# Performance work log

Measured on AMD Instinct MI355X. Metric: run time of the kernel, lower is better.

The kernel has to match this reference:

```python
import jax, jax.numpy as jnp
import numpy as np

N = 50000
E = 640000
H = 128


def setup_inputs() -> dict:
    key = jax.random.key(0)
    ks = jax.random.split(key, 16)
    s = 0.02
    return {
        "x": jax.random.uniform(ks[0], (N, 1), dtype=jnp.float32),
        "pre_h": jax.random.normal(ks[1], (N, H), dtype=jnp.float32),
        "edge_index": jax.random.randint(ks[2], (2, E), 0, N, dtype=jnp.int32),
        "edge_attr": jax.random.uniform(ks[3], (E, 1), dtype=jnp.float32),
        # encoder: Linear(1+H, H)
        "W_enc": jax.random.normal(ks[4], (1 + H, H), dtype=jnp.float32) * s,
        "b_enc": jnp.zeros((H,), dtype=jnp.float32),
        # message: Linear(2H+1, H)
        "W_M": jax.random.normal(ks[5], (2 * H + 1, H), dtype=jnp.float32) * s,
        "b_M": jnp.zeros((H,), dtype=jnp.float32),
        # update: Linear(2H, H)
        "W_U": jax.random.normal(ks[6], (2 * H, H), dtype=jnp.float32) * s,
        "b_U": jnp.zeros((H,), dtype=jnp.float32),
        # decoder: Linear(2H, 1)
        "W_dec": jax.random.normal(ks[7], (2 * H, 1), dtype=jnp.float32) * s,
        "b_dec": jnp.zeros((1,), dtype=jnp.float32),
        # terminator: Linear(2H, 1)
        "W_term": jax.random.normal(ks[8], (2 * H, 1), dtype=jnp.float32) * s,
        "b_term": jnp.zeros((1,), dtype=jnp.float32),
    }


def reference(x, pre_h, edge_index, edge_attr,
              W_enc, b_enc, W_M, b_M, W_U, b_U,
              W_dec, b_dec, W_term, b_term):
    n = x.shape[0]
    # Encoder: z = relu(Linear([x, pre_h]))  -> [N, H]
    z = jax.nn.relu(jnp.concatenate([x, pre_h], axis=-1) @ W_enc + b_enc)

    # MPNN processor (PyG flow source_to_target: row=src j, col=dst i)
    src, dst = edge_index[0], edge_index[1]
    z_i = z[dst]  # [E, H]
    z_j = z[src]  # [E, H]
    m = jax.nn.relu(jnp.concatenate([z_i, z_j, edge_attr], axis=-1) @ W_M + b_M)
    agg = jax.ops.segment_max(m, dst, num_segments=n)
    # PyG fills nodes with no incoming edges with 0 for max aggregation;
    # messages are >= 0 (relu) so clamping at 0 matches exactly.
    agg = jnp.maximum(agg, jnp.float32(0.0))
    h = jax.nn.relu(jnp.concatenate([z, agg], axis=-1) @ W_U + b_U)

    # Decoder: y = Linear([z, h]) -> [N, 1]
    y = jnp.concatenate([z, h], axis=-1) @ W_dec + b_dec

    # Terminator
    h_mean = jnp.mean(h, axis=0, keepdims=True)              # [1, H]
    hm = jnp.broadcast_to(h_mean, h.shape)                   # [N, H]
    t = jnp.concatenate([h, hm], axis=-1) @ W_term + b_term  # [N, 1]
    tau = jnp.mean(t, axis=0, keepdims=True)                 # [1, 1]

    return h, y, tau
```

## Files before the change

kernel.cpp:

```cpp
#include <hip/hip_runtime.h>

#define DEVINL __device__ __forceinline__
#define BCAP 64
#define NREP 64

typedef __attribute__((ext_vector_type(8))) short short8;
typedef __attribute__((ext_vector_type(4))) float f32x4;
typedef __attribute__((ext_vector_type(4))) unsigned short ushort4v;

DEVINL unsigned short f2bf(float f) {
    unsigned u = __float_as_uint(f);
    u += 0x7fffu + ((u >> 16) & 1u);
    return (unsigned short)(u >> 16);
}
DEVINL float bf2f(unsigned short s) { return __uint_as_float(((unsigned)s) << 16); }

__global__ __launch_bounds__(256) void k_w(
    const float* __restrict__ Wenc, const float* __restrict__ WM,
    const float* __restrict__ WU,
    unsigned short* __restrict__ WencT, unsigned short* __restrict__ WM1T,
    unsigned short* __restrict__ WM2T, unsigned short* __restrict__ WUT,
    int* __restrict__ zbase, int zn)
{
    if (blockIdx.x < 64) {
        int tid = blockIdx.x * 256 + threadIdx.x;
        const int nt = 64 * 256;
        for (int i = tid; i < 128 * 128; i += nt) {
            int c = i >> 7, k = i & 127;
            WencT[c * 128 + k] = f2bf(Wenc[(1 + k) * 128 + c]);
            WM1T[c * 128 + k]  = f2bf(WM[k * 128 + c]);
            WM2T[c * 128 + k]  = f2bf(WM[(128 + k) * 128 + c]);
        }
        for (int i = tid; i < 128 * 256; i += nt) {
            int c = i >> 8, k = i & 255;
            WUT[c * 256 + k] = f2bf(WU[k * 128 + c]);
        }
    } else {
        for (int i = (blockIdx.x - 64) * 256 + threadIdx.x; i < zn; i += 32 * 256)
            zbase[i] = 0;
    }
}


__global__ __launch_bounds__(256) void k_zq(
    const float* __restrict__ x, const float* __restrict__ preh,
    const unsigned short* __restrict__ WencT, const float* __restrict__ Wenc,
    const float* __restrict__ benc, const unsigned short* __restrict__ WM2T,
    unsigned short* __restrict__ zb, unsigned short* __restrict__ Qb,
    int N, int nzq,
    const int* __restrict__ ei, const float* __restrict__ attr,
    int* __restrict__ cnt, int2* __restrict__ bucket, int E)
{
    if ((int)blockIdx.x >= nzq) {
        int e = ((int)blockIdx.x - nzq) * 256 + threadIdx.x;
        if (e >= E) return;
        int src = ei[e];
        int dst = ei[E + e];
        float a = attr[e];
        int slot = atomicAdd(&cnt[dst], 1);
        if (slot < BCAP)
            bucket[(size_t)dst * BCAP + slot] = make_int2(src, __float_as_int(a));
        return;
    }
    __shared__ __align__(16) unsigned short zl[16][136];
    int t = threadIdx.x;
    int wave = t >> 6, lane = t & 63;
    int m = lane & 15, quad = lane >> 4;
    int node = (int)blockIdx.x * 16 + m;
    bool valid = node < N;
    int nodec = min(node, N - 1);
    f32x4 acc[2] = {(f32x4)0.f, (f32x4)0.f};
    const float* arow = preh + (size_t)nodec * 128;
#pragma unroll
    for (int kc = 0; kc < 4; ++kc) {
        int k0 = kc * 32 + quad * 8;
        float4 f0 = *(const float4*)(arow + k0);
        float4 f1 = *(const float4*)(arow + k0 + 4);
        short8 bfrag;
        bfrag[0] = (short)f2bf(f0.x); bfrag[1] = (short)f2bf(f0.y);
        bfrag[2] = (short)f2bf(f0.z); bfrag[3] = (short)f2bf(f0.w);
        bfrag[4] = (short)f2bf(f1.x); bfrag[5] = (short)f2bf(f1.y);
        bfrag[6] = (short)f2bf(f1.z); bfrag[7] = (short)f2bf(f1.w);
#pragma unroll
        for (int tt = 0; tt < 2; ++tt) {
            int t8 = wave * 2 + tt;
            short8 afrag = *(const short8*)(WencT + (size_t)(t8 * 16 + m) * 128 + k0);
            acc[tt] = __builtin_amdgcn_mfma_f32_16x16x32_bf16(afrag, bfrag, acc[tt], 0, 0, 0);
        }
    }
    float xv = x[nodec];
#pragma unroll
    for (int tt = 0; tt < 2; ++tt) {
        int col = (wave * 2 + tt) * 16 + quad * 4;
        float4 w0v = *(const float4*)(Wenc + col);
        float4 bv  = *(const float4*)(benc + col);
        ushort4v o;
        o[0] = f2bf(fmaxf(acc[tt][0] + xv * w0v.x + bv.x, 0.f));
        o[1] = f2bf(fmaxf(acc[tt][1] + xv * w0v.y + bv.y, 0.f));
        o[2] = f2bf(fmaxf(acc[tt][2] + xv * w0v.z + bv.z, 0.f));
        o[3] = f2bf(fmaxf(acc[tt][3] + xv * w0v.w + bv.w, 0.f));
        if (valid) *(ushort4v*)(zb + (size_t)node * 128 + col) = o;
        *(ushort4v*)&zl[m][col] = o;
    }
    __syncthreads();
    f32x4 aQ[2] = {(f32x4)0.f, (f32x4)0.f};
#pragma unroll
    for (int kc = 0; kc < 4; ++kc) {
        int k0 = kc * 32 + quad * 8;
        short8 bfrag = *(const short8*)&zl[m][k0];
#pragma unroll
        for (int tt = 0; tt < 2; ++tt) {
            int t8 = wave * 2 + tt;
            short8 a2 = *(const short8*)(WM2T + (size_t)(t8 * 16 + m) * 128 + k0);
            aQ[tt] = __builtin_amdgcn_mfma_f32_16x16x32_bf16(a2, bfrag, aQ[tt], 0, 0, 0);
        }
    }
    if (!valid) return;
    unsigned short* qrow = Qb + (size_t)node * 128;
#pragma unroll
    for (int tt = 0; tt < 2; ++tt) {
        int col = (wave * 2 + tt) * 16 + quad * 4;
        ushort4v oq;
        oq[0] = f2bf(aQ[tt][0]); oq[1] = f2bf(aQ[tt][1]);
        oq[2] = f2bf(aQ[tt][2]); oq[3] = f2bf(aQ[tt][3]);
        *(ushort4v*)(qrow + col) = oq;
    }
}

__global__ __launch_bounds__(256) void k_aggh(
    const unsigned short* __restrict__ zb, const unsigned short* __restrict__ Qb,
    const int2* __restrict__ bucket, const int* __restrict__ cnt,
    const float* __restrict__ w3, const float* __restrict__ bM,
    const unsigned short* __restrict__ WUT, const unsigned short* __restrict__ WM1T,
    const float* __restrict__ bU, const float* __restrict__ Wd,
    const float* __restrict__ bd,
    float* __restrict__ h, float* __restrict__ y, float* __restrict__ hsumR,
    int N)
{
    __shared__ int degs[16];
    __shared__ __align__(16) int2 eb[16][BCAP];
    __shared__ __align__(16) float mac[16][132];
    __shared__ float ys[4][16];
    __shared__ float hsb[128];
    unsigned short (*al)[136] = (unsigned short (*)[136])eb;

    int t = threadIdx.x;
    int bid16 = (int)blockIdx.x * 16;
    int wave = t >> 6, lane = t & 63;
    int m = lane & 15, quad = lane >> 4;
    int node = bid16 + m;
    bool valid = node < N;
    int nodec = min(node, N - 1);

    const unsigned short* arow = zb + (size_t)nodec * 128;
    short8 zfr[4];
#pragma unroll
    for (int kc = 0; kc < 4; ++kc)
        zfr[kc] = *(const short8*)(arow + kc * 32 + quad * 8);

    if (t < 16) degs[t] = min(cnt[min(bid16 + t, N - 1)], BCAP);
    __syncthreads();
    for (int idx = t; idx < 16 * BCAP; idx += 256) {
        int nd = idx >> 6, sl = idx & (BCAP - 1);
        if (sl < degs[nd])
            eb[nd][sl] = bucket[(size_t)min(bid16 + nd, N - 1) * BCAP + sl];
    }
    __syncthreads();
    {
        int il = t >> 4, c0 = (t & 15) * 8;
        int deg = degs[il];
        float w[8];
        {
            float4 wa = *(const float4*)(w3 + c0), wb = *(const float4*)(w3 + c0 + 4);
            w[0]=wa.x; w[1]=wa.y; w[2]=wa.z; w[3]=wa.w;
            w[4]=wb.x; w[5]=wb.y; w[6]=wb.z; w[7]=wb.w;
        }
        const float NI = __uint_as_float(0xff800000u);
        float a8[8];
#pragma unroll
        for (int u = 0; u < 8; ++u) a8[u] = NI;
        int j = 0;
        for (; j + 7 < deg; j += 8) {
            int2 e[8]; short8 q[8];
#pragma unroll
            for (int b = 0; b < 8; ++b) e[b] = eb[il][j + b];
#pragma unroll
            for (int b = 0; b < 8; ++b)
                q[b] = *(const short8*)(Qb + (size_t)e[b].x * 128 + c0);
#pragma unroll
            for (int b = 0; b < 8; ++b) {
                float a = __int_as_float(e[b].y);
#pragma unroll
                for (int u = 0; u < 8; ++u)
                    a8[u] = fmaxf(a8[u], fmaf(a, w[u], bf2f((unsigned short)q[b][u])));
            }
        }
        for (; j + 3 < deg; j += 4) {
            int2 e[4]; short8 q[4];
#pragma unroll
            for (int b = 0; b < 4; ++b) e[b] = eb[il][j + b];
#pragma unroll
            for (int b = 0; b < 4; ++b)
                q[b] = *(const short8*)(Qb + (size_t)e[b].x * 128 + c0);
#pragma unroll
            for (int b = 0; b < 4; ++b) {
                float a = __int_as_float(e[b].y);
#pragma unroll
                for (int u = 0; u < 8; ++u)
                    a8[u] = fmaxf(a8[u], fmaf(a, w[u], bf2f((unsigned short)q[b][u])));
            }
        }
        for (; j < deg; ++j) {
            int2 e0 = eb[il][j];
            float a = __int_as_float(e0.y);
            short8 q0 = *(const short8*)(Qb + (size_t)e0.x * 128 + c0);
#pragma unroll
            for (int u = 0; u < 8; ++u)
                a8[u] = fmaxf(a8[u], fmaf(a, w[u], bf2f((unsigned short)q0[u])));
        }
        *(f32x4*)&mac[il][c0]     = *(f32x4*)&a8[0];
        *(f32x4*)&mac[il][c0 + 4] = *(f32x4*)&a8[4];
    }
    __syncthreads();
    {
        f32x4 accP[2] = {(f32x4)0.f, (f32x4)0.f};
#pragma unroll
        for (int kc = 0; kc < 4; ++kc) {
            int k0 = kc * 32 + quad * 8;
#pragma unroll
            for (int tt = 0; tt < 2; ++tt) {
                int t8 = wave * 2 + tt;
                short8 afrag = *(const short8*)(WM1T + (size_t)(t8 * 16 + m) * 128 + k0);
                accP[tt] = __builtin_amdgcn_mfma_f32_16x16x32_bf16(afrag, zfr[kc], accP[tt], 0, 0, 0);
            }
        }
#pragma unroll
        for (int tt = 0; tt < 2; ++tt) {
            int col = (wave * 2 + tt) * 16 + quad * 4;
            float4 bmv = *(const float4*)(bM + col);
            float4 mv  = *(const float4*)&mac[m][col];
            ushort4v o;
            o[0] = f2bf(fmaxf(accP[tt][0] + bmv.x + mv.x, 0.f));
            o[1] = f2bf(fmaxf(accP[tt][1] + bmv.y + mv.y, 0.f));
            o[2] = f2bf(fmaxf(accP[tt][2] + bmv.z + mv.z, 0.f));
            o[3] = f2bf(fmaxf(accP[tt][3] + bmv.w + mv.w, 0.f));
            *(ushort4v*)&al[m][col] = o;
        }
    }
    __syncthreads();
    f32x4 acc[2] = {(f32x4)0.f, (f32x4)0.f};
    float py = 0.f;
#pragma unroll
    for (int kc = 0; kc < 8; ++kc) {
        int k0 = kc * 32 + quad * 8;
        short8 bfrag;
        if (kc < 4) {
            bfrag = zfr[kc];
            if (wave == 0) {
                float4 wa = *(const float4*)(Wd + k0);
                float4 wb = *(const float4*)(Wd + k0 + 4);
                py += bf2f((unsigned short)bfrag[0]) * wa.x
                    + bf2f((unsigned short)bfrag[1]) * wa.y
                    + bf2f((unsigned short)bfrag[2]) * wa.z
                    + bf2f((unsigned short)bfrag[3]) * wa.w
                    + bf2f((unsigned short)bfrag[4]) * wb.x
                    + bf2f((unsigned short)bfrag[5]) * wb.y
                    + bf2f((unsigned short)bfrag[6]) * wb.z
                    + bf2f((unsigned short)bfrag[7]) * wb.w;
            }
        } else {
            bfrag = *(const short8*)&al[m][(kc - 4) * 32 + quad * 8];
        }
#pragma unroll
        for (int tt = 0; tt < 2; ++tt) {
            int t8 = wave * 2 + tt;
            short8 afrag = *(const short8*)(WUT + (size_t)(t8 * 16 + m) * 256 + k0);
            acc[tt] = __builtin_amdgcn_mfma_f32_16x16x32_bf16(afrag, bfrag, acc[tt], 0, 0, 0);
        }
    }
    const float* Wdh = Wd + 128;
    float* orow = h + (size_t)nodec * 128;
#pragma unroll
    for (int tt = 0; tt < 2; ++tt) {
        int col = (wave * 2 + tt) * 16 + quad * 4;
        float4 bv = *(const float4*)(bU + col);
        float4 o;
        o.x = valid ? fmaxf(acc[tt][0] + bv.x, 0.f) : 0.f;
        o.y = valid ? fmaxf(acc[tt][1] + bv.y, 0.f) : 0.f;
        o.z = valid ? fmaxf(acc[tt][2] + bv.z, 0.f) : 0.f;
        o.w = valid ? fmaxf(acc[tt][3] + bv.w, 0.f) : 0.f;
        if (valid) *(float4*)(orow + col) = o;
        float4 wd = *(const float4*)(Wdh + col);
        py += o.x * wd.x + o.y * wd.y + o.z * wd.z + o.w * wd.w;
        float4 s = o;
#pragma unroll
        for (int mask = 1; mask <= 8; mask <<= 1) {
            s.x += __shfl_xor(s.x, mask, 64);
            s.y += __shfl_xor(s.y, mask, 64);
            s.z += __shfl_xor(s.z, mask, 64);
            s.w += __shfl_xor(s.w, mask, 64);
        }
        if (m == 0) *(float4*)&hsb[col] = s;
    }
    py += __shfl_xor(py, 16, 64);
    py += __shfl_xor(py, 32, 64);
    if (lane < 16) ys[wave][lane] = py;
    __syncthreads();
    if (t < 16 && bid16 + t < N)
        y[bid16 + t] = ys[0][t] + ys[1][t] + ys[2][t] + ys[3][t] + bd[0];
    if (t < 128)
        atomicAdd(&hsumR[((int)blockIdx.x & (NREP - 1)) * 128 + t], hsb[t]);
}

__global__ __launch_bounds__(128) void k_tau(
    const float* __restrict__ hsumR, const float* __restrict__ Wt,
    const float* __restrict__ bt, float* __restrict__ tau, int N)
{
    __shared__ float sd[128];
    int t = threadIdx.x;
    float s = 0.f;
#pragma unroll
    for (int r = 0; r < NREP; ++r) s += hsumR[r * 128 + t];
    float v = s * (1.f / (float)N) * (Wt[t] + Wt[128 + t]);
    sd[t] = v;
    __syncthreads();
    for (int o = 64; o > 0; o >>= 1) {
        if (t < o) sd[t] += sd[t + o];
        __syncthreads();
    }
    if (t == 0) tau[0] = sd[0] + bt[0];
}

extern "C" void kernel_launch(void* const* d_in, const int* in_sizes, int n_in,
                              void* d_out, int out_size, void* d_ws, size_t ws_size,
                              hipStream_t stream)
{
    const float* x     = (const float*)d_in[0];
    const float* preh  = (const float*)d_in[1];
    const int*   ei    = (const int*)d_in[2];
    const float* attr  = (const float*)d_in[3];
    const float* Wenc  = (const float*)d_in[4];
    const float* benc  = (const float*)d_in[5];
    const float* WM    = (const float*)d_in[6];
    const float* bM    = (const float*)d_in[7];
    const float* WU    = (const float*)d_in[8];
    const float* bU    = (const float*)d_in[9];
    const float* Wd    = (const float*)d_in[10];
    const float* bd    = (const float*)d_in[11];
    const float* Wterm = (const float*)d_in[12];
    const float* bterm = (const float*)d_in[13];
    int N = in_sizes[0];
    int E = in_sizes[3];

    char* wp = (char*)d_ws;
    unsigned short* zb    = (unsigned short*)wp; wp += (size_t)N * 128 * 2;
    unsigned short* Qb    = (unsigned short*)wp; wp += (size_t)N * 128 * 2;
    int2*           bucket= (int2*)wp;           wp += (size_t)N * BCAP * 8;
    int*            cnt   = (int*)wp;            wp += (size_t)N * 4;
    float*          hsumR = (float*)wp;          wp += NREP * 128 * 4;
    unsigned short* WencT = (unsigned short*)wp; wp += 128 * 128 * 2;
    unsigned short* WM1T  = (unsigned short*)wp; wp += 128 * 128 * 2;
    unsigned short* WM2T  = (unsigned short*)wp; wp += 128 * 128 * 2;
    unsigned short* WUT   = (unsigned short*)wp; wp += 128 * 256 * 2;

    float* hout = (float*)d_out;
    float* yout = hout + (size_t)N * 128;
    float* tau  = yout + N;

    int nb16 = (N + 15) / 16;
    int sb = (E + 255) / 256;
    int zn = N + NREP * 128;

    k_w<<<96, 256, 0, stream>>>(Wenc, WM, WU, WencT, WM1T, WM2T, WUT,
                                cnt, zn);
    k_zq<<<nb16 + sb, 256, 0, stream>>>(x, preh, WencT, Wenc, benc, WM2T,
                                        zb, Qb, N, nb16,
                                        ei, attr, cnt, bucket, E);
    k_aggh<<<nb16, 256, 0, stream>>>(zb, Qb, bucket, cnt, WM + 256 * 128, bM,
                                     WUT, WM1T, bU, Wd, bd,
                                     hout, yout, hsumR, N);
    k_tau<<<1, 128, 0, stream>>>(hsumR, Wterm, bterm, tau, N);
}
```

Baseline: 260.0 us.

## Pack edge buckets into 32-bit entries and move scatter into prep kernel

Edge bucket entries are packed into one 32-bit word (16-bit source index plus a bf16 edge attribute) instead of an int2. This halves bucket write and read traffic and the shared-memory staging size. The edge scatter moves from the z/Q kernel into the weight-prep kernel, and counter zeroing becomes a memset. In exchange, source indices above 65535 are unsupported and edge_attr is rounded to bf16, and an extra barrier is added because the output staging aliases the smaller edge buffer.

```diff
diff --git a/kernel.cpp b/kernel.cpp
--- a/kernel.cpp
+++ b/kernel.cpp
@@ -15,12 +15,13 @@
 }
 DEVINL float bf2f(unsigned short s) { return __uint_as_float(((unsigned)s) << 16); }
 
-__global__ __launch_bounds__(256) void k_w(
+__global__ __launch_bounds__(256) void k_prep(
     const float* __restrict__ Wenc, const float* __restrict__ WM,
     const float* __restrict__ WU,
     unsigned short* __restrict__ WencT, unsigned short* __restrict__ WM1T,
     unsigned short* __restrict__ WM2T, unsigned short* __restrict__ WUT,
-    int* __restrict__ zbase, int zn)
+    const int* __restrict__ ei, const float* __restrict__ attr,
+    int* __restrict__ cnt, unsigned* __restrict__ bucket, int E)
 {
     if (blockIdx.x < 64) {
         int tid = blockIdx.x * 256 + threadIdx.x;
@@ -36,32 +37,24 @@
             WUT[c * 256 + k] = f2bf(WU[k * 128 + c]);
         }
     } else {
-        for (int i = (blockIdx.x - 64) * 256 + threadIdx.x; i < zn; i += 32 * 256)
-            zbase[i] = 0;
-    }
-}
-
-
-__global__ __launch_bounds__(256) void k_zq(
-    const float* __restrict__ x, const float* __restrict__ preh,
-    const unsigned short* __restrict__ WencT, const float* __restrict__ Wenc,
-    const float* __restrict__ benc, const unsigned short* __restrict__ WM2T,
-    unsigned short* __restrict__ zb, unsigned short* __restrict__ Qb,
-    int N, int nzq,
-    const int* __restrict__ ei, const float* __restrict__ attr,
-    int* __restrict__ cnt, int2* __restrict__ bucket, int E)
-{
-    if ((int)blockIdx.x >= nzq) {
-        int e = ((int)blockIdx.x - nzq) * 256 + threadIdx.x;
+        int e = ((int)blockIdx.x - 64) * 256 + threadIdx.x;
         if (e >= E) return;
         int src = ei[e];
         int dst = ei[E + e];
         float a = attr[e];
         int slot = atomicAdd(&cnt[dst], 1);
         if (slot < BCAP)
-            bucket[(size_t)dst * BCAP + slot] = make_int2(src, __float_as_int(a));
-        return;
-    }
+            bucket[(size_t)dst * BCAP + slot] = ((unsigned)src << 16) | f2bf(a);
+    }
+}
+
+
+__global__ __launch_bounds__(256) void k_zq(
+    const float* __restrict__ x, const float* __restrict__ preh,
+    const unsigned short* __restrict__ WencT, const float* __restrict__ Wenc,
+    const float* __restrict__ benc, const unsigned short* __restrict__ WM2T,
+    unsigned short* __restrict__ zb, unsigned short* __restrict__ Qb, int N)
+{
     __shared__ __align__(16) unsigned short zl[16][136];
     int t = threadIdx.x;
     int wave = t >> 6, lane = t & 63;
@@ -129,7 +122,7 @@
 
 __global__ __launch_bounds__(256) void k_aggh(
     const unsigned short* __restrict__ zb, const unsigned short* __restrict__ Qb,
-    const int2* __restrict__ bucket, const int* __restrict__ cnt,
+    const unsigned* __restrict__ bucket, const int* __restrict__ cnt,
     const float* __restrict__ w3, const float* __restrict__ bM,
     const unsigned short* __restrict__ WUT, const unsigned short* __restrict__ WM1T,
     const float* __restrict__ bU, const float* __restrict__ Wd,
@@ -138,7 +131,7 @@
     int N)
 {
     __shared__ int degs[16];
-    __shared__ __align__(16) int2 eb[16][BCAP];
+    __shared__ __align__(16) unsigned eb[16][68];
     __shared__ __align__(16) float mac[16][132];
     __shared__ float ys[4][16];
     __shared__ float hsb[128];
@@ -181,39 +174,39 @@
         for (int u = 0; u < 8; ++u) a8[u] = NI;
         int j = 0;
         for (; j + 7 < deg; j += 8) {
-            int2 e[8]; short8 q[8];
+            unsigned e[8]; short8 q[8];
 #pragma unroll
             for (int b = 0; b < 8; ++b) e[b] = eb[il][j + b];
 #pragma unroll
             for (int b = 0; b < 8; ++b)
-                q[b] = *(const short8*)(Qb + (size_t)e[b].x * 128 + c0);
+                q[b] = *(const short8*)(Qb + (size_t)(e[b] >> 16) * 128 + c0);
 #pragma unroll
             for (int b = 0; b < 8; ++b) {
-                float a = __int_as_float(e[b].y);
+                float a = bf2f((unsigned short)(e[b] & 0xffffu));
 #pragma unroll
                 for (int u = 0; u < 8; ++u)
                     a8[u] = fmaxf(a8[u], fmaf(a, w[u], bf2f((unsigned short)q[b][u])));
             }
         }
         for (; j + 3 < deg; j += 4) {
-            int2 e[4]; short8 q[4];
+            unsigned e[4]; short8 q[4];
 #pragma unroll
             for (int b = 0; b < 4; ++b) e[b] = eb[il][j + b];
 #pragma unroll
             for (int b = 0; b < 4; ++b)
-                q[b] = *(const short8*)(Qb + (size_t)e[b].x * 128 + c0);
+                q[b] = *(const short8*)(Qb + (size_t)(e[b] >> 16) * 128 + c0);
 #pragma unroll
             for (int b = 0; b < 4; ++b) {
-                float a = __int_as_float(e[b].y);
+                float a = bf2f((unsigned short)(e[b] & 0xffffu));
 #pragma unroll
                 for (int u = 0; u < 8; ++u)
                     a8[u] = fmaxf(a8[u], fmaf(a, w[u], bf2f((unsigned short)q[b][u])));
             }
         }
         for (; j < deg; ++j) {
-            int2 e0 = eb[il][j];
-            float a = __int_as_float(e0.y);
-            short8 q0 = *(const short8*)(Qb + (size_t)e0.x * 128 + c0);
+            unsigned e0 = eb[il][j];
+            float a = bf2f((unsigned short)(e0 & 0xffffu));
+            short8 q0 = *(const short8*)(Qb + (size_t)(e0 >> 16) * 128 + c0);
 #pragma unroll
             for (int u = 0; u < 8; ++u)
                 a8[u] = fmaxf(a8[u], fmaf(a, w[u], bf2f((unsigned short)q0[u])));
@@ -234,6 +227,7 @@
                 accP[tt] = __builtin_amdgcn_mfma_f32_16x16x32_bf16(afrag, zfr[kc], accP[tt], 0, 0, 0);
             }
         }
+        __syncthreads();
 #pragma unroll
         for (int tt = 0; tt < 2; ++tt) {
             int col = (wave * 2 + tt) * 16 + quad * 4;
@@ -355,7 +349,7 @@
     char* wp = (char*)d_ws;
     unsigned short* zb    = (unsigned short*)wp; wp += (size_t)N * 128 * 2;
     unsigned short* Qb    = (unsigned short*)wp; wp += (size_t)N * 128 * 2;
-    int2*           bucket= (int2*)wp;           wp += (size_t)N * BCAP * 8;
+    unsigned*       bucket= (unsigned*)wp;       wp += (size_t)N * BCAP * 4;
     int*            cnt   = (int*)wp;            wp += (size_t)N * 4;
     float*          hsumR = (float*)wp;          wp += NREP * 128 * 4;
     unsigned short* WencT = (unsigned short*)wp; wp += 128 * 128 * 2;
@@ -369,13 +363,12 @@
 
     int nb16 = (N + 15) / 16;
     int sb = (E + 255) / 256;
-    int zn = N + NREP * 128;
-
-    k_w<<<96, 256, 0, stream>>>(Wenc, WM, WU, WencT, WM1T, WM2T, WUT,
-                                cnt, zn);
-    k_zq<<<nb16 + sb, 256, 0, stream>>>(x, preh, WencT, Wenc, benc, WM2T,
-                                        zb, Qb, N, nb16,
+
+    hipMemsetAsync(cnt, 0, ((size_t)N + NREP * 128) * sizeof(int), stream);
+    k_prep<<<64 + sb, 256, 0, stream>>>(Wenc, WM, WU, WencT, WM1T, WM2T, WUT,
                                         ei, attr, cnt, bucket, E);
+    k_zq<<<nb16, 256, 0, stream>>>(x, preh, WencT, Wenc, benc, WM2T,
+                                   zb, Qb, N);
     k_aggh<<<nb16, 256, 0, stream>>>(zb, Qb, bucket, cnt, WM + 256 * 128, bM,
                                      WUT, WM1T, bU, Wd, bd,
                                      hout, yout, hsumR, N);
```

Measured after the change: 251.7 us. 1.03x faster.
